# Kernel tuning notes

Hardware: AMD Instinct MI355X
Metric: run time of the kernel (lower is better)

## Reference

```python
import jax, jax.numpy as jnp
import numpy as np

D_MODEL = 1024
NUM_HEADS = 16
D_K = D_MODEL // NUM_HEADS
D_FF = 4096


def setup_inputs() -> dict:
    key = jax.random.key(0)
    ks = jax.random.split(key, 12)
    s = 1.0 / np.sqrt(D_MODEL)
    sf = 1.0 / np.sqrt(D_FF)
    return {
        "x": jax.random.normal(ks[0], (2, 2048, D_MODEL), dtype=jnp.float32),
        # nn.Linear weights are [out_features, in_features]
        "Wq": jax.random.uniform(ks[1], (D_MODEL, D_MODEL), jnp.float32, -s, s),
        "Wk": jax.random.uniform(ks[2], (D_MODEL, D_MODEL), jnp.float32, -s, s),
        "Wv": jax.random.uniform(ks[3], (D_MODEL, D_MODEL), jnp.float32, -s, s),
        "Wo": jax.random.uniform(ks[4], (D_MODEL, D_MODEL), jnp.float32, -s, s),
        "W1": jax.random.uniform(ks[5], (D_FF, D_MODEL), jnp.float32, -s, s),
        "W2": jax.random.uniform(ks[6], (D_MODEL, D_FF), jnp.float32, -sf, sf),
        "g1": jnp.ones((D_MODEL,), jnp.float32),
        "b1": jnp.zeros((D_MODEL,), jnp.float32),
        "g2": jnp.ones((D_MODEL,), jnp.float32),
        "b2": jnp.zeros((D_MODEL,), jnp.float32),
    }


def _layer_norm(x, gamma, beta, eps=1e-5):
    mu = jnp.mean(x, axis=-1, keepdims=True)
    var = jnp.mean((x - mu) ** 2, axis=-1, keepdims=True)
    return (x - mu) * jax.lax.rsqrt(var + eps) * gamma + beta


def reference(x, Wq, Wk, Wv, Wo, W1, W2, g1, b1, g2, b2):
    B, S, _ = x.shape
    H, Dk = NUM_HEADS, D_K
    # projections (Linear: x @ W.T), split heads -> [B, H, S, Dk]
    q = (x @ Wq.T).reshape(B, S, H, Dk).transpose(0, 2, 1, 3)
    k = (x @ Wk.T).reshape(B, S, H, Dk).transpose(0, 2, 1, 3)
    v = (x @ Wv.T).reshape(B, S, H, Dk).transpose(0, 2, 1, 3)
    scores = jnp.einsum('bhsd,bhtd->bhst', q, k) / jnp.sqrt(jnp.float32(Dk))
    attn = jax.nn.softmax(scores, axis=-1)
    out = jnp.einsum('bhst,bhtd->bhsd', attn, v)
    out = out.transpose(0, 2, 1, 3).reshape(B, S, H * Dk)
    out = out @ Wo.T
    x_after_attn = _layer_norm(x + out, g1, b1)
    ff = jax.nn.gelu(x_after_attn @ W1.T, approximate=False)
    ff_out = ff @ W2.T
    return _layer_norm(x_after_attn + ff_out, g2, b2)
```

## Files before the change

kernel.cpp:

```cpp
#include <hip/hip_runtime.h>
#include <hip/hip_bf16.h>
#include <cstdint>
#include <cstddef>

#define D_MODEL 1024
#define D_FF    4096
#define NTOK    4096
#define SEQ     2048
#define NH      16
#define DK      64
#define LDQ     3072

typedef __bf16 bf16;
typedef __bf16 bf16_8 __attribute__((ext_vector_type(8)));
typedef __bf16 bf16_4 __attribute__((ext_vector_type(4)));
typedef float  f32_4  __attribute__((ext_vector_type(4)));

__device__ __forceinline__ void async_copy16(const bf16* g, bf16* l) {
    __builtin_amdgcn_global_load_lds((const __attribute__((address_space(1))) void*)g,
                                     (__attribute__((address_space(3))) void*)l,
                                     16, 0, 0);
}

__global__ __launch_bounds__(256)
void cast_all(const float* __restrict__ x,  const float* __restrict__ Wq,
              const float* __restrict__ Wk, const float* __restrict__ Wv,
              const float* __restrict__ Wo, const float* __restrict__ W1,
              const float* __restrict__ W2,
              bf16* __restrict__ xb, bf16* __restrict__ Wqkvb,
              bf16* __restrict__ Wob, bf16* __restrict__ W1b,
              bf16* __restrict__ W2b) {
    const int blk = blockIdx.x;
    const float* s; bf16* d; int off;
    if (blk < 4096)       { s = x;  d = xb;              off = blk; }
    else if (blk < 5120)  { s = Wq; d = Wqkvb;           off = blk - 4096; }
    else if (blk < 6144)  { s = Wk; d = Wqkvb + 1048576; off = blk - 5120; }
    else if (blk < 7168)  { s = Wv; d = Wqkvb + 2097152; off = blk - 6144; }
    else if (blk < 8192)  { s = Wo; d = Wob;             off = blk - 7168; }
    else if (blk < 12288) { s = W1; d = W1b;             off = blk - 8192; }
    else                  { s = W2; d = W2b;             off = blk - 12288; }
    const int i = off * 1024 + threadIdx.x * 4;
    float4 v = *(const float4*)(s + i);
    bf16_4 o;
    o[0] = (bf16)v.x; o[1] = (bf16)v.y; o[2] = (bf16)v.z; o[3] = (bf16)v.w;
    *(bf16_4*)(d + i) = o;
}

template <int EPI>
__global__ __launch_bounds__(256, 2)
void gemm_bt(const bf16* __restrict__ A, const bf16* __restrict__ B,
             bf16* __restrict__ C0, size_t cstride,
             int M, int N, int ldk, int kLen) {
    __shared__ bf16 As[128 * 32];
    __shared__ bf16 Bs[128 * 32];
    const int tid  = threadIdx.x;
    const int wave = tid >> 6, lane = tid & 63;
    const int quad = lane >> 4, l15 = lane & 15;
    const int wm = wave >> 1, wn = wave & 1;
    const int bm = blockIdx.x, bn = blockIdx.y, z = blockIdx.z;

    const bf16* A0 = A + (size_t)bm * 128 * ldk + (size_t)z * kLen;
    const bf16* B0 = B + (size_t)bn * 128 * ldk + (size_t)z * kLen;

    f32_4 acc[4][4];
#pragma unroll
    for (int i = 0; i < 4; i++)
#pragma unroll
        for (int j = 0; j < 4; j++) acc[i][j] = (f32_4){0.f, 0.f, 0.f, 0.f};

    const int ra = tid >> 2;
    const int gl = (tid & 3) ^ ((ra >> 1) & 3);
    const int ca = gl * 8;
    const int sx = (l15 >> 1) & 3;

    for (int k0 = 0; k0 < kLen; k0 += 32) {
#pragma unroll
        for (int c = 0; c < 2; c++)
            async_copy16(&A0[(size_t)(c * 64 + ra) * ldk + k0 + ca],
                         &As[c * 2048 + wave * 512]);
#pragma unroll
        for (int c = 0; c < 2; c++)
            async_copy16(&B0[(size_t)(c * 64 + ra) * ldk + k0 + ca],
                         &Bs[c * 2048 + wave * 512]);
        __syncthreads();

        bf16_8 af[4], bfr[4];
#pragma unroll
        for (int mi = 0; mi < 4; mi++)
            af[mi] = *(const bf16_8*)&As[(wm * 64 + mi * 16 + l15) * 32 + ((quad ^ sx) * 8)];
#pragma unroll
        for (int ni = 0; ni < 4; ni++)
            bfr[ni] = *(const bf16_8*)&Bs[(wn * 64 + ni * 16 + l15) * 32 + ((quad ^ sx) * 8)];
#pragma unroll
        for (int mi = 0; mi < 4; mi++)
#pragma unroll
            for (int ni = 0; ni < 4; ni++)
                acc[mi][ni] = __builtin_amdgcn_mfma_f32_16x16x32_bf16(
                    af[mi], bfr[ni], acc[mi][ni], 0, 0, 0);
        __syncthreads();
    }

    bf16* C = C0 + (size_t)z * cstride;
    const int row0 = bm * 128 + wm * 64 + quad * 4;
    const int col0 = bn * 128 + wn * 64 + l15;
#pragma unroll
    for (int mi = 0; mi < 4; mi++) {
#pragma unroll
        for (int ni = 0; ni < 4; ni++) {
#pragma unroll
            for (int r = 0; r < 4; r++) {
                int row = row0 + mi * 16 + r;
                int col = col0 + ni * 16;
                size_t idx = (size_t)row * N + col;
                float v = acc[mi][ni][r];
                if (EPI == 0) {
                    C[idx] = (bf16)v;
                } else {
                    float g = 0.5f * v * (1.0f + erff(v * 0.70710678118654752f));
                    C[idx] = (bf16)g;
                }
            }
        }
    }
}

__global__ __launch_bounds__(256)
void transpose_v(const bf16* __restrict__ QKV, bf16* __restrict__ Vt) {
    __shared__ bf16 T[64 * 72];
    const int tb = blockIdx.x;
    const int cb = blockIdx.y;
    const int tid = threadIdx.x;
    const int r = tid >> 3, g = tid & 7;
#pragma unroll
    for (int c = 0; c < 2; ++c) {
        int row = c * 32 + r;
        bf16_8 v = *(const bf16_8*)&QKV[(size_t)(tb * 64 + row) * LDQ + 2048 + cb * 64 + g * 8];
        *(bf16_8*)&T[row * 72 + g * 8] = v;
    }
    __syncthreads();
    const int b  = (tb * 64) >> 11;
    const int s0 = (tb * 64) & 2047;
#pragma unroll
    for (int c = 0; c < 2; ++c) {
        int ch = c * 32 + r;
        bf16_8 v;
#pragma unroll
        for (int j = 0; j < 8; ++j) v[j] = T[(g * 8 + j) * 72 + ch];
        *(bf16_8*)&Vt[(size_t)(b * 1024 + cb * 64 + ch) * SEQ + s0 + g * 8] = v;
    }
}

__global__ __launch_bounds__(256)
void attn4(const bf16* __restrict__ QKV, const bf16* __restrict__ Vt,
           bf16* __restrict__ O) {
    __shared__ bf16 Ks[64 * 64];
    __shared__ bf16 Vs[64 * 64];
    __shared__ bf16 Ps[4][32 * 64];

    const int tid  = threadIdx.x;
    const int wave = tid >> 6, lane = tid & 63;
    const int quad = lane >> 4, l15 = lane & 15;
    const int qb = blockIdx.x & 15;
    const int h  = (blockIdx.x >> 4) & 15;
    const int b  = blockIdx.x >> 8;

    const bf16* Qg = QKV + (size_t)(b * SEQ) * LDQ + h * 64;
    const bf16* Kg = QKV + (size_t)(b * SEQ) * LDQ + 1024 + h * 64;
    const bf16* Vg = Vt + (size_t)(b * 1024 + h * 64) * SEQ;

    const int q0 = qb * 128 + wave * 32;
    bf16_8 qf[2][2];
#pragma unroll
    for (int qg = 0; qg < 2; qg++)
#pragma unroll
        for (int j = 0; j < 2; j++)
            qf[qg][j] = *(const bf16_8*)&Qg[(size_t)(q0 + qg * 16 + l15) * LDQ + j * 32 + quad * 8];

    const int srow = wave * 8 + (lane >> 3);
    const int sg   = lane & 7;
    const int xl   = l15 & 7;

    float l_s[2] = {0.f, 0.f};
    f32_4 o_acc[2][4];
#pragma unroll
    for (int qg = 0; qg < 2; qg++)
#pragma unroll
        for (int d = 0; d < 4; d++) o_acc[qg][d] = (f32_4){0.f, 0.f, 0.f, 0.f};

    bf16* P = Ps[wave];

    for (int t = 0; t < SEQ / 64; ++t) {
        const int k0 = t * 64;
        __syncthreads();
#pragma unroll
        for (int c = 0; c < 2; ++c) {
            int r = c * 32 + srow;
            async_copy16(&Kg[(size_t)(k0 + r) * LDQ + ((sg ^ (r & 7)) * 8)],
                         &Ks[c * 2048 + wave * 512]);
            async_copy16(&Vg[(size_t)r * SEQ + k0 + ((sg ^ (r & 7)) * 8)],
                         &Vs[c * 2048 + wave * 512]);
        }
        __syncthreads();

        f32_4 s[2][4];
#pragma unroll
        for (int ni = 0; ni < 4; ni++) {
            const bf16* kp = &Ks[(ni * 16 + l15) * 64];
            bf16_8 kb0 = *(const bf16_8*)&kp[(quad ^ xl) * 8];
            bf16_8 kb1 = *(const bf16_8*)&kp[((quad + 4) ^ xl) * 8];
#pragma unroll
            for (int qg = 0; qg < 2; qg++) {
                f32_4 z = (f32_4){0.f, 0.f, 0.f, 0.f};
                z = __builtin_amdgcn_mfma_f32_16x16x32_bf16(kb0, qf[qg][0], z, 0, 0, 0);
                s[qg][ni] = __builtin_amdgcn_mfma_f32_16x16x32_bf16(kb1, qf[qg][1], z, 0, 0, 0);
            }
        }

#pragma unroll
        for (int qg = 0; qg < 2; qg++)
#pragma unroll
            for (int ni = 0; ni < 4; ni++) {
                bf16_4 pk;
#pragma unroll
                for (int r = 0; r < 4; r++) {
                    float p = exp2f(fmaf(s[qg][ni][r], 0.18033688011112042f,
                                         -11.541560327111707f));
                    l_s[qg] += p;
                    pk[r] = (bf16)p;
                }
                int G = ni * 2 + (quad >> 1);
                *(bf16_4*)&P[(qg * 16 + l15) * 64 + ((G ^ xl) * 8) + ((quad & 1) * 4)] = pk;
            }
        bf16_8 pf[2][2];
#pragma unroll
        for (int qg = 0; qg < 2; qg++) {
            pf[qg][0] = *(const bf16_8*)&P[(qg * 16 + l15) * 64 + ((quad ^ xl) * 8)];
            pf[qg][1] = *(const bf16_8*)&P[(qg * 16 + l15) * 64 + (((quad + 4) ^ xl) * 8)];
        }

#pragma unroll
        for (int dt = 0; dt < 4; dt++) {
            const bf16* vp = &Vs[(dt * 16 + l15) * 64];
            bf16_8 vb0 = *(const bf16_8*)&vp[(quad ^ xl) * 8];
            bf16_8 vb1 = *(const bf16_8*)&vp[((quad + 4) ^ xl) * 8];
#pragma unroll
            for (int qg = 0; qg < 2; qg++) {
                o_acc[qg][dt] = __builtin_amdgcn_mfma_f32_16x16x32_bf16(
                    vb0, pf[qg][0], o_acc[qg][dt], 0, 0, 0);
                o_acc[qg][dt] = __builtin_amdgcn_mfma_f32_16x16x32_bf16(
                    vb1, pf[qg][1], o_acc[qg][dt], 0, 0, 0);
            }
        }
    }

#pragma unroll
    for (int qg = 0; qg < 2; qg++) {
        l_s[qg] += __shfl_xor(l_s[qg], 16);
        l_s[qg] += __shfl_xor(l_s[qg], 32);
        l_s[qg] = 1.0f / l_s[qg];
    }

#pragma unroll
    for (int qg = 0; qg < 2; qg++)
#pragma unroll
        for (int dt = 0; dt < 4; dt++) {
            bf16_4 pk;
#pragma unroll
            for (int r = 0; r < 4; r++) pk[r] = (bf16)(o_acc[qg][dt][r] * l_s[qg]);
            int G = dt * 2 + (quad >> 1);
            *(bf16_4*)&P[(qg * 16 + l15) * 64 + ((G ^ xl) * 8) + ((quad & 1) * 4)] = pk;
        }
#pragma unroll
    for (int pass = 0; pass < 4; pass++) {
        int rowl = pass * 8 + (lane >> 3);
        int g = lane & 7;
        bf16_8 ov = *(const bf16_8*)&P[rowl * 64 + ((g ^ (rowl & 7)) * 8)];
        size_t grow = (size_t)b * SEQ + qb * 128 + wave * 32 + rowl;
        *(bf16_8*)&O[grow * D_MODEL + h * 64 + g * 8] = ov;
    }
}

template <bool A32, bool O32>
__global__ __launch_bounds__(256)
void ln_kernel(const void* __restrict__ av, const bf16* __restrict__ p0,
               const bf16* __restrict__ p1, const bf16* __restrict__ p2,
               const bf16* __restrict__ p3,
               const float* __restrict__ gamma, const float* __restrict__ beta,
               void* __restrict__ yv) {
    const int row = blockIdx.x;
    const int tid = threadIdx.x;
    const size_t off = (size_t)row * D_MODEL;
    float v[4];
    {
        bf16_4 a0 = *(const bf16_4*)(p0 + off + tid * 4);
        bf16_4 a1 = *(const bf16_4*)(p1 + off + tid * 4);
        bf16_4 a2 = *(const bf16_4*)(p2 + off + tid * 4);
        bf16_4 a3 = *(const bf16_4*)(p3 + off + tid * 4);
        if (A32) {
            float4 xa = *(const float4*)((const float*)av + off + tid * 4);
            v[0] = xa.x; v[1] = xa.y; v[2] = xa.z; v[3] = xa.w;
        } else {
            bf16_4 xa = *(const bf16_4*)((const bf16*)av + off + tid * 4);
#pragma unroll
            for (int i = 0; i < 4; i++) v[i] = (float)xa[i];
        }
#pragma unroll
        for (int i = 0; i < 4; i++)
            v[i] += ((float)a0[i] + (float)a1[i]) + ((float)a2[i] + (float)a3[i]);
    }
    float s = v[0] + v[1] + v[2] + v[3];
    float ss = v[0] * v[0] + v[1] * v[1] + v[2] * v[2] + v[3] * v[3];
#pragma unroll
    for (int m = 1; m < 64; m <<= 1) {
        s  += __shfl_xor(s, m);
        ss += __shfl_xor(ss, m);
    }
    __shared__ float red_s[4], red_q[4];
    int wave = tid >> 6, lane = tid & 63;
    if (lane == 0) { red_s[wave] = s; red_q[wave] = ss; }
    __syncthreads();
    s  = red_s[0] + red_s[1] + red_s[2] + red_s[3];
    ss = red_q[0] + red_q[1] + red_q[2] + red_q[3];
    float mu   = s * (1.f / D_MODEL);
    float var  = ss * (1.f / D_MODEL) - mu * mu;
    float rstd = rsqrtf(var + 1e-5f);
    float4 gg = *(const float4*)(gamma + tid * 4);
    float4 be = *(const float4*)(beta + tid * 4);
    float y0 = (v[0] - mu) * rstd * gg.x + be.x;
    float y1 = (v[1] - mu) * rstd * gg.y + be.y;
    float y2 = (v[2] - mu) * rstd * gg.z + be.z;
    float y3 = (v[3] - mu) * rstd * gg.w + be.w;
    if (O32) {
        *(float4*)((float*)yv + off + tid * 4) = make_float4(y0, y1, y2, y3);
    } else {
        bf16_4 o;
        o[0] = (bf16)y0; o[1] = (bf16)y1; o[2] = (bf16)y2; o[3] = (bf16)y3;
        *(bf16_4*)((bf16*)yv + off + tid * 4) = o;
    }
}

extern "C" void kernel_launch(void* const* d_in, const int* in_sizes, int n_in,
                              void* d_out, int out_size, void* d_ws, size_t ws_size,
                              hipStream_t stream) {
    (void)in_sizes; (void)n_in; (void)out_size; (void)ws_size;
    const float* x  = (const float*)d_in[0];
    const float* Wq = (const float*)d_in[1];
    const float* Wk = (const float*)d_in[2];
    const float* Wv = (const float*)d_in[3];
    const float* Wo = (const float*)d_in[4];
    const float* W1 = (const float*)d_in[5];
    const float* W2 = (const float*)d_in[6];
    const float* g1 = (const float*)d_in[7];
    const float* b1 = (const float*)d_in[8];
    const float* g2 = (const float*)d_in[9];
    const float* b2 = (const float*)d_in[10];

    char* ws = (char*)d_ws;
    bf16*  xb    = (bf16*)(ws + 0);
    bf16*  aob   = xb;
    bf16*  ln1b  = (bf16*)(ws + 0);
    bf16*  QKVb  = (bf16*)(ws + 8388608);
    bf16*  Vtb   = (bf16*)(ws + 33554432);
    bf16*  hb    = (bf16*)(ws + 8388608);
    bf16*  Wqkvb = (bf16*)(ws + 41943040);
    bf16*  Wob   = (bf16*)(ws + 48234496);
    bf16*  W1b   = (bf16*)(ws + 50331648);
    bf16*  W2b   = (bf16*)(ws + 58720256);
    bf16*  proj0 = (bf16*)(ws + 67108864);
    const size_t PSTRIDE = (size_t)NTOK * D_MODEL;

    cast_all<<<dim3(16384), 256, 0, stream>>>(x, Wq, Wk, Wv, Wo, W1, W2,
                                              xb, Wqkvb, Wob, W1b, W2b);

    gemm_bt<0><<<dim3(NTOK / 128, 3072 / 128, 1), 256, 0, stream>>>(
        xb, Wqkvb, QKVb, 0, NTOK, 3072, D_MODEL, D_MODEL);

    transpose_v<<<dim3(NTOK / 64, D_MODEL / 64), 256, 0, stream>>>(QKVb, Vtb);

    attn4<<<dim3(512), 256, 0, stream>>>(QKVb, Vtb, aob);

    gemm_bt<0><<<dim3(NTOK / 128, D_MODEL / 128, 4), 256, 0, stream>>>(
        aob, Wob, proj0, PSTRIDE, NTOK, D_MODEL, D_MODEL, 256);
    ln_kernel<true, false><<<NTOK, 256, 0, stream>>>(
        x, proj0, proj0 + PSTRIDE, proj0 + 2 * PSTRIDE, proj0 + 3 * PSTRIDE,
        g1, b1, ln1b);

    gemm_bt<2><<<dim3(NTOK / 128, D_FF / 128, 1), 256, 0, stream>>>(
        ln1b, W1b, hb, 0, NTOK, D_FF, D_MODEL, D_MODEL);

    gemm_bt<0><<<dim3(NTOK / 128, D_MODEL / 128, 4), 256, 0, stream>>>(
        hb, W2b, proj0, PSTRIDE, NTOK, D_MODEL, D_FF, 1024);
    ln_kernel<false, true><<<NTOK, 256, 0, stream>>>(
        ln1b, proj0, proj0 + PSTRIDE, proj0 + 2 * PSTRIDE, proj0 + 3 * PSTRIDE,
        g2, b2, d_out);
}
```

Before: 348.3 us.

## Rewrite attention with 32x32 MFMA, split-K across waves, register-held P

The attention kernel moves from 16x16x32 to 32x32x16 bf16 MFMA tiles. Each block now handles 64 queries over 128-key tiles, with two waves splitting the keys and merging partial outputs and row sums through shared memory at the end. The softmax probabilities are rearranged into B-operand fragments with cross-lane shuffles instead of a round trip through LDS, and the grid doubles to 1024 blocks for better occupancy across CUs. The trade-off is a final reduction step, extra shared memory and higher register pressure from the 32x32 accumulators.

```diff
diff --git a/kernel.cpp b/kernel.cpp
--- a/kernel.cpp
+++ b/kernel.cpp
@@ -15,6 +15,7 @@
 typedef __bf16 bf16_8 __attribute__((ext_vector_type(8)));
 typedef __bf16 bf16_4 __attribute__((ext_vector_type(4)));
 typedef float  f32_4  __attribute__((ext_vector_type(4)));
+typedef float  f32_16 __attribute__((ext_vector_type(16)));
 
 __device__ __forceinline__ void async_copy16(const bf16* g, bf16* l) {
     __builtin_amdgcn_global_load_lds((const __attribute__((address_space(1))) void*)g,
@@ -151,132 +152,145 @@
 }
 
 __global__ __launch_bounds__(256)
-void attn4(const bf16* __restrict__ QKV, const bf16* __restrict__ Vt,
+void attn5(const bf16* __restrict__ QKV, const bf16* __restrict__ Vt,
            bf16* __restrict__ O) {
-    __shared__ bf16 Ks[64 * 64];
-    __shared__ bf16 Vs[64 * 64];
-    __shared__ bf16 Ps[4][32 * 64];
+    __shared__ __align__(16) bf16 SM[128 * 64 + 64 * 128];
+    __shared__ float Lsh[4][32];
+    bf16* Ks = SM;
+    bf16* Vs = SM + 128 * 64;
 
     const int tid  = threadIdx.x;
     const int wave = tid >> 6, lane = tid & 63;
-    const int quad = lane >> 4, l15 = lane & 15;
-    const int qb = blockIdx.x & 15;
-    const int h  = (blockIdx.x >> 4) & 15;
-    const int b  = blockIdx.x >> 8;
+    const int ln31 = lane & 31, hi = lane >> 5;
+    const int qh = wave >> 1, kh = wave & 1;
+    const int qb = blockIdx.x & 31;
+    const int h  = (blockIdx.x >> 5) & 15;
+    const int b  = blockIdx.x >> 9;
 
     const bf16* Qg = QKV + (size_t)(b * SEQ) * LDQ + h * 64;
     const bf16* Kg = QKV + (size_t)(b * SEQ) * LDQ + 1024 + h * 64;
     const bf16* Vg = Vt + (size_t)(b * 1024 + h * 64) * SEQ;
 
-    const int q0 = qb * 128 + wave * 32;
-    bf16_8 qf[2][2];
-#pragma unroll
-    for (int qg = 0; qg < 2; qg++)
-#pragma unroll
-        for (int j = 0; j < 2; j++)
-            qf[qg][j] = *(const bf16_8*)&Qg[(size_t)(q0 + qg * 16 + l15) * LDQ + j * 32 + quad * 8];
-
-    const int srow = wave * 8 + (lane >> 3);
-    const int sg   = lane & 7;
-    const int xl   = l15 & 7;
-
-    float l_s[2] = {0.f, 0.f};
-    f32_4 o_acc[2][4];
-#pragma unroll
-    for (int qg = 0; qg < 2; qg++)
-#pragma unroll
-        for (int d = 0; d < 4; d++) o_acc[qg][d] = (f32_4){0.f, 0.f, 0.f, 0.f};
-
-    bf16* P = Ps[wave];
-
-    for (int t = 0; t < SEQ / 64; ++t) {
-        const int k0 = t * 64;
+    const int q0 = qb * 64 + qh * 32;
+    bf16_8 qf[4];
+#pragma unroll
+    for (int c = 0; c < 4; c++)
+        qf[c] = *(const bf16_8*)&Qg[(size_t)(q0 + ln31) * LDQ + c * 16 + hi * 8];
+
+    f32_16 o0, o1;
+#pragma unroll
+    for (int r = 0; r < 16; r++) { o0[r] = 0.f; o1[r] = 0.f; }
+    float l_lane = 0.f;
+
+    const int krow_s = wave * 8 + (lane >> 3);
+    const int kg_s   = lane & 7;
+    const int vrow_s = wave * 4 + (lane >> 4);
+    const int vg_s   = lane & 15;
+
+    for (int t = 0; t < SEQ / 128; ++t) {
+        const int k0 = t * 128;
         __syncthreads();
 #pragma unroll
-        for (int c = 0; c < 2; ++c) {
-            int r = c * 32 + srow;
-            async_copy16(&Kg[(size_t)(k0 + r) * LDQ + ((sg ^ (r & 7)) * 8)],
-                         &Ks[c * 2048 + wave * 512]);
-            async_copy16(&Vg[(size_t)r * SEQ + k0 + ((sg ^ (r & 7)) * 8)],
-                         &Vs[c * 2048 + wave * 512]);
+        for (int i = 0; i < 4; ++i) {
+            int r = i * 32 + krow_s;
+            async_copy16(&Kg[(size_t)(k0 + r) * LDQ + ((kg_s ^ (r & 7)) * 8)],
+                         &Ks[(i * 32 + wave * 8) * 64]);
+        }
+#pragma unroll
+        for (int i = 0; i < 4; ++i) {
+            int r = i * 16 + vrow_s;
+            async_copy16(&Vg[(size_t)r * SEQ + k0 + ((vg_s ^ ((r & 7) << 1)) * 8)],
+                         &Vs[(i * 16 + wave * 4) * 128]);
         }
         __syncthreads();
 
-        f32_4 s[2][4];
-#pragma unroll
-        for (int ni = 0; ni < 4; ni++) {
-            const bf16* kp = &Ks[(ni * 16 + l15) * 64];
-            bf16_8 kb0 = *(const bf16_8*)&kp[(quad ^ xl) * 8];
-            bf16_8 kb1 = *(const bf16_8*)&kp[((quad + 4) ^ xl) * 8];
-#pragma unroll
-            for (int qg = 0; qg < 2; qg++) {
-                f32_4 z = (f32_4){0.f, 0.f, 0.f, 0.f};
-                z = __builtin_amdgcn_mfma_f32_16x16x32_bf16(kb0, qf[qg][0], z, 0, 0, 0);
-                s[qg][ni] = __builtin_amdgcn_mfma_f32_16x16x32_bf16(kb1, qf[qg][1], z, 0, 0, 0);
+        float p[2][16];
+#pragma unroll
+        for (int kt = 0; kt < 2; kt++) {
+            const int krow = kh * 64 + kt * 32 + ln31;
+            f32_16 acc;
+#pragma unroll
+            for (int r = 0; r < 16; r++) acc[r] = 0.f;
+#pragma unroll
+            for (int c = 0; c < 4; c++) {
+                bf16_8 kf = *(const bf16_8*)&Ks[krow * 64 + (((2 * c + hi) ^ (krow & 7)) * 8)];
+                acc = __builtin_amdgcn_mfma_f32_32x32x16_bf16(kf, qf[c], acc, 0, 0, 0);
             }
-        }
-
-#pragma unroll
-        for (int qg = 0; qg < 2; qg++)
-#pragma unroll
-            for (int ni = 0; ni < 4; ni++) {
-                bf16_4 pk;
-#pragma unroll
-                for (int r = 0; r < 4; r++) {
-                    float p = exp2f(fmaf(s[qg][ni][r], 0.18033688011112042f,
-                                         -11.541560327111707f));
-                    l_s[qg] += p;
-                    pk[r] = (bf16)p;
+#pragma unroll
+            for (int r = 0; r < 16; r++) {
+                float pp = exp2f(fmaf(acc[r], 0.18033688011112042f,
+                                      -11.541560327111707f));
+                l_lane += pp;
+                p[kt][r] = pp;
+            }
+        }
+
+        bf16_8 pfrag[4];
+#pragma unroll
+        for (int kc = 0; kc < 4; kc++) {
+            const float* pp = p[kc >> 1] + 8 * (kc & 1);
+            bf16_8 f;
+#pragma unroll
+            for (int j = 0; j < 4; j++) {
+                float t0 = hi ? pp[j] : pp[j + 4];
+                float rc = __shfl_xor(t0, 32);
+                f[j]     = (bf16)(hi ? rc : pp[j]);
+                f[4 + j] = (bf16)(hi ? pp[j + 4] : rc);
+            }
+            pfrag[kc] = f;
+        }
+
+#pragma unroll
+        for (int kc = 0; kc < 4; kc++) {
+            const int g = kh * 8 + kc * 2 + hi;
+            bf16_8 vf0 = *(const bf16_8*)&Vs[ln31 * 128 + ((g ^ ((ln31 & 7) << 1)) * 8)];
+            o0 = __builtin_amdgcn_mfma_f32_32x32x16_bf16(vf0, pfrag[kc], o0, 0, 0, 0);
+            const int vr1 = 32 + ln31;
+            bf16_8 vf1 = *(const bf16_8*)&Vs[vr1 * 128 + ((g ^ ((vr1 & 7) << 1)) * 8)];
+            o1 = __builtin_amdgcn_mfma_f32_32x32x16_bf16(vf1, pfrag[kc], o1, 0, 0, 0);
+        }
+    }
+
+    l_lane += __shfl_xor(l_lane, 32);
+
+    __syncthreads();
+    float* Osh = (float*)SM;
+    if (kh == 1) {
+        float* pub = Osh + qh * 2048;
+#pragma unroll
+        for (int r = 0; r < 16; r++) {
+            pub[r * 64 + lane]         = o0[r];
+            pub[(16 + r) * 64 + lane]  = o1[r];
+        }
+    }
+    if (hi == 0) Lsh[wave][ln31] = l_lane;
+    __syncthreads();
+    if (kh == 0) {
+        const float* pub = Osh + qh * 2048;
+        float L = Lsh[wave][ln31] + Lsh[wave + 1][ln31];
+        float rl = 1.0f / L;
+        bf16* ob = (bf16*)(Osh + 4096 + qh * 1024);
+#pragma unroll
+        for (int dt = 0; dt < 2; dt++)
+#pragma unroll
+            for (int g = 0; g < 4; g++) {
+                bf16_4 w;
+#pragma unroll
+                for (int jj = 0; jj < 4; jj++) {
+                    int r = g * 4 + jj;
+                    float own = dt ? o1[r] : o0[r];
+                    w[jj] = (bf16)((own + pub[(dt * 16 + r) * 64 + lane]) * rl);
                 }
-                int G = ni * 2 + (quad >> 1);
-                *(bf16_4*)&P[(qg * 16 + l15) * 64 + ((G ^ xl) * 8) + ((quad & 1) * 4)] = pk;
+                *(bf16_4*)&ob[ln31 * 64 + (((dt * 4 + g) ^ (ln31 & 7)) * 8) + hi * 4] = w;
             }
-        bf16_8 pf[2][2];
-#pragma unroll
-        for (int qg = 0; qg < 2; qg++) {
-            pf[qg][0] = *(const bf16_8*)&P[(qg * 16 + l15) * 64 + ((quad ^ xl) * 8)];
-            pf[qg][1] = *(const bf16_8*)&P[(qg * 16 + l15) * 64 + (((quad + 4) ^ xl) * 8)];
-        }
-
-#pragma unroll
-        for (int dt = 0; dt < 4; dt++) {
-            const bf16* vp = &Vs[(dt * 16 + l15) * 64];
-            bf16_8 vb0 = *(const bf16_8*)&vp[(quad ^ xl) * 8];
-            bf16_8 vb1 = *(const bf16_8*)&vp[((quad + 4) ^ xl) * 8];
-#pragma unroll
-            for (int qg = 0; qg < 2; qg++) {
-                o_acc[qg][dt] = __builtin_amdgcn_mfma_f32_16x16x32_bf16(
-                    vb0, pf[qg][0], o_acc[qg][dt], 0, 0, 0);
-                o_acc[qg][dt] = __builtin_amdgcn_mfma_f32_16x16x32_bf16(
-                    vb1, pf[qg][1], o_acc[qg][dt], 0, 0, 0);
-            }
-        }
-    }
-
-#pragma unroll
-    for (int qg = 0; qg < 2; qg++) {
-        l_s[qg] += __shfl_xor(l_s[qg], 16);
-        l_s[qg] += __shfl_xor(l_s[qg], 32);
-        l_s[qg] = 1.0f / l_s[qg];
-    }
-
-#pragma unroll
-    for (int qg = 0; qg < 2; qg++)
-#pragma unroll
-        for (int dt = 0; dt < 4; dt++) {
-            bf16_4 pk;
-#pragma unroll
-            for (int r = 0; r < 4; r++) pk[r] = (bf16)(o_acc[qg][dt][r] * l_s[qg]);
-            int G = dt * 2 + (quad >> 1);
-            *(bf16_4*)&P[(qg * 16 + l15) * 64 + ((G ^ xl) * 8) + ((quad & 1) * 4)] = pk;
-        }
-#pragma unroll
-    for (int pass = 0; pass < 4; pass++) {
-        int rowl = pass * 8 + (lane >> 3);
-        int g = lane & 7;
-        bf16_8 ov = *(const bf16_8*)&P[rowl * 64 + ((g ^ (rowl & 7)) * 8)];
-        size_t grow = (size_t)b * SEQ + qb * 128 + wave * 32 + rowl;
-        *(bf16_8*)&O[grow * D_MODEL + h * 64 + g * 8] = ov;
+#pragma unroll
+        for (int pass = 0; pass < 4; pass++) {
+            int qr = pass * 8 + (lane >> 3);
+            int lg = lane & 7;
+            bf16_8 ov = *(const bf16_8*)&ob[qr * 64 + ((lg ^ (qr & 7)) * 8)];
+            size_t tok = (size_t)b * SEQ + qb * 64 + qh * 32 + qr;
+            *(bf16_8*)&O[tok * D_MODEL + h * 64 + lg * 8] = ov;
+        }
     }
 }
 
@@ -377,7 +391,7 @@
 
     transpose_v<<<dim3(NTOK / 64, D_MODEL / 64), 256, 0, stream>>>(QKVb, Vtb);
 
-    attn4<<<dim3(512), 256, 0, stream>>>(QKVb, Vtb, aob);
+    attn5<<<dim3(1024), 256, 0, stream>>>(QKVb, Vtb, aob);
 
     gemm_bt<0><<<dim3(NTOK / 128, D_MODEL / 128, 4), 256, 0, stream>>>(
         aob, Wob, proj0, PSTRIDE, NTOK, D_MODEL, D_MODEL, 256);
```

Measured after the change: 369.9 us. 1.06x slower.
